# Optimization experiments

Measured on AMD Instinct MI355X. Metric: run time of the kernel, lower is better.

## Reference

```python
import jax, jax.numpy as jnp
import numpy as np

B, S, D, H = 2, 2048, 1024, 16
DK = D // H
NEG = -1e9


def setup_inputs() -> dict:
    key = jax.random.key(0)
    ks = jax.random.split(key, 12)
    scale = 1.0 / np.sqrt(D)
    inp = {
        'Q': jax.random.normal(ks[0], (B, S, D), jnp.float32),
        'K': jax.random.normal(ks[1], (B, S, D), jnp.float32),
        'V': jax.random.normal(ks[2], (B, S, D), jnp.float32),
        'mask': jnp.tril(jnp.ones((S, S), jnp.int32))[None, None],  # (1,1,S,S) causal
        # torch nn.Linear layout: W has shape (out, in), y = x @ W.T + b
        'WQ': jax.random.normal(ks[3], (D, D), jnp.float32) * scale,
        'bQ': jnp.zeros((D,), jnp.float32),
        'WK': jax.random.normal(ks[4], (D, D), jnp.float32) * scale,
        'bK': jnp.zeros((D,), jnp.float32),
        'WV': jax.random.normal(ks[5], (D, D), jnp.float32) * scale,
        'bV': jnp.zeros((D,), jnp.float32),
        'WO': jax.random.normal(ks[6], (D, D), jnp.float32) * scale,
        'bO': jnp.zeros((D,), jnp.float32),
    }
    return inp


def reference(Q, K, V, mask, WQ, bQ, WK, bK, WV, bV, WO, bO):
    # projections (torch Linear: x @ W.T + b), then split heads -> (B,H,S,DK)
    def split_heads(x):
        return x.reshape(B, S, H, DK).transpose(0, 2, 1, 3)

    Qh = split_heads(Q @ WQ.T + bQ)
    Kh = split_heads(K @ WK.T + bK)
    Vh = split_heads(V @ WV.T + bV)

    scores = jnp.einsum('bhqd,bhkd->bhqk', Qh, Kh) / jnp.sqrt(jnp.float32(DK))
    scores = jnp.where(mask == 0, NEG, scores)
    attn = jax.nn.softmax(scores, axis=-1)  # (B,H,S,S)
    ctx = jnp.einsum('bhqk,bhkd->bhqd', attn, Vh)
    concat = ctx.transpose(0, 2, 1, 3).reshape(B, S, D)
    out = concat @ WO.T + bO
    return out, attn
```

## Files before the change

kernel.cpp:

```cpp
#include <hip/hip_runtime.h>
#include <hip/hip_bf16.h>
#include <cstdint>
#include <cstddef>

#define S_ 2048
#define D_ 1024
#define H_ 16
#define DK_ 64
#define B_ 2

typedef unsigned short u16;
typedef __attribute__((ext_vector_type(8))) short bf16x8;
typedef __attribute__((ext_vector_type(4))) float f32x4;

__device__ inline u16 f2bf(float f) {
    union { float f; unsigned u; } c; c.f = f;
    unsigned u = c.u;
    unsigned r = (u + 0x7fffu + ((u >> 16) & 1u)) >> 16;
    return (u16)r;
}

__device__ inline uint4 cvt8(const float* __restrict__ src) {
    float4 f0 = *(const float4*)(src);
    float4 f1 = *(const float4*)(src + 4);
    union { u16 h[8]; uint4 v; } u;
    u.h[0] = f2bf(f0.x); u.h[1] = f2bf(f0.y); u.h[2] = f2bf(f0.z); u.h[3] = f2bf(f0.w);
    u.h[4] = f2bf(f1.x); u.h[5] = f2bf(f1.y); u.h[6] = f2bf(f1.z); u.h[7] = f2bf(f1.w);
    return u.v;
}

__device__ inline unsigned pkbf(float a, float b) {
    unsigned r;
    asm("v_cvt_pk_bf16_f32 %0, %1, %2" : "=v"(r) : "v"(a), "v"(b));
    return r;
}

typedef __attribute__((address_space(3))) void lds_void;
typedef __attribute__((address_space(1))) const void glob_void;
__device__ __forceinline__ void glds16(const u16* g, u16* l, int lane) {
#if __has_builtin(__builtin_amdgcn_global_load_lds)
    (void)lane;
    __builtin_amdgcn_global_load_lds((glob_void*)g, (lds_void*)l, 16, 0, 0);
#else
    ((uint4*)l)[lane] = *(const uint4*)g;
#endif
}

__device__ __forceinline__ bf16x8 rd64(const u16* arr, int row, int k) {
    return *(const bf16x8*)((const char*)arr + (row << 7)
             + ((k << 1) ^ ((row & 7) << 4)));
}
__device__ __forceinline__ bf16x8 rd128(const u16* arr, int row, int k) {
    return *(const bf16x8*)((const char*)arr + (row << 8)
             + ((k << 1) ^ ((row & 7) << 4)));
}

__global__ void __launch_bounds__(256)
cvt_all(const float* __restrict__ Q, const float* __restrict__ K,
        const float* __restrict__ V,
        const float* __restrict__ WQ, const float* __restrict__ WK,
        const float* __restrict__ WV, const float* __restrict__ WO,
        u16* __restrict__ Qb, u16* __restrict__ Kb, u16* __restrict__ Vb,
        u16* __restrict__ Wb)
{
    const size_t QN = 524288;
    const size_t WN = 131072;
    size_t u = (size_t)blockIdx.x * 256 + threadIdx.x;
    const size_t total = 3 * QN + 4 * WN;
    const size_t stride = (size_t)gridDim.x * 256;
    for (; u < total; u += stride) {
        const float* s; u16* d; size_t off;
        if (u < 3 * QN) {
            size_t seg = u / QN;
            off = (u - seg * QN) << 3;
            s = (seg == 0) ? Q : (seg == 1) ? K : V;
            d = (seg == 0) ? Qb : (seg == 1) ? Kb : Vb;
        } else {
            size_t w = u - 3 * QN;
            size_t seg = w / WN;
            off = (w - seg * WN) << 3;
            s = (seg == 0) ? WQ : (seg == 1) ? WK : (seg == 2) ? WV : WO;
            d = Wb + seg * 1048576;
        }
        *(uint4*)&d[off] = cvt8(s + off);
    }
}

__device__ __forceinline__ void gemm_core(
    const u16* __restrict__ A, const u16* __restrict__ Bm,
    int m0, int n0, int tid, u16* As, u16* Bs, f32x4 (&acc)[4][4])
{
    const int lane = tid & 63;
    const int wave = tid >> 6;
    const int wm = wave >> 1, wn = wave & 1;
    const int fr = lane & 15, fq = lane >> 4;

    for (int k0 = 0; k0 < 1024; k0 += 64) {
        __syncthreads();
#pragma unroll
        for (int it = 0; it < 4; ++it) {
            int linear = it * 256 + tid;
            int row = linear >> 3, c = linear & 7;
            glds16(&A[(size_t)(m0 + row) * 1024 + k0 + ((c ^ (row & 7)) << 3)],
                   &As[(size_t)(it * 256 + (tid & ~63)) << 3], lane);
        }
#pragma unroll
        for (int it = 0; it < 4; ++it) {
            int linear = it * 256 + tid;
            int row = linear >> 3, c = linear & 7;
            glds16(&Bm[(size_t)(n0 + row) * 1024 + k0 + ((c ^ (row & 7)) << 3)],
                   &Bs[(size_t)(it * 256 + (tid & ~63)) << 3], lane);
        }
        __syncthreads();
#pragma unroll
        for (int ks = 0; ks < 64; ks += 32) {
            bf16x8 af[4], bfv[4];
#pragma unroll
            for (int mt = 0; mt < 4; ++mt)
                af[mt] = rd64(As, wm * 64 + mt * 16 + fr, ks + (fq << 3));
#pragma unroll
            for (int nt = 0; nt < 4; ++nt)
                bfv[nt] = rd64(Bs, wn * 64 + nt * 16 + fr, ks + (fq << 3));
#pragma unroll
            for (int mt = 0; mt < 4; ++mt)
#pragma unroll
                for (int nt = 0; nt < 4; ++nt)
                    acc[mt][nt] = __builtin_amdgcn_mfma_f32_16x16x32_bf16(
                        bfv[nt], af[mt], acc[mt][nt], 0, 0, 0);
        }
    }
}

__global__ void __launch_bounds__(256)
proj_qkv(const u16* __restrict__ Qb, const u16* __restrict__ Kb,
         const u16* __restrict__ Vb, const u16* __restrict__ Wb,
         const float* __restrict__ bQ, const float* __restrict__ bK,
         const float* __restrict__ bV,
         u16* __restrict__ Qh, u16* __restrict__ Kh, u16* __restrict__ Vt)
{
    __shared__ __align__(16) u16 As[128 * 64];
    __shared__ __align__(16) u16 Bs[128 * 64];

    const int tid  = threadIdx.x;
    const int lane = tid & 63;
    const int wave = tid >> 6;
    const int wm = wave >> 1, wn = wave & 1;
    const int fr = lane & 15, fq = lane >> 4;
    const int m0 = blockIdx.y * 128;
    const int n0 = blockIdx.x * 128;
    const int z  = blockIdx.z;

    const u16* A = (z == 0) ? Qb : (z == 1) ? Kb : Vb;
    const u16* W = Wb + (size_t)z * 1048576;
    const float* bias = (z == 0) ? bQ : (z == 1) ? bK : bV;
    u16* O = (z == 0) ? Qh : (z == 1) ? Kh : Vt;

    f32x4 acc[4][4];
#pragma unroll
    for (int i = 0; i < 4; ++i)
#pragma unroll
        for (int j = 0; j < 4; ++j) acc[i][j] = (f32x4){0.f, 0.f, 0.f, 0.f};

    gemm_core(A, W, m0, n0, tid, As, Bs, acc);

#pragma unroll
    for (int mt = 0; mt < 4; ++mt) {
#pragma unroll
        for (int nt = 0; nt < 4; ++nt) {
            int row  = m0 + wm * 64 + mt * 16 + fr;
            int colb = n0 + wn * 64 + nt * 16 + (fq << 2);
            float4 b4 = *(const float4*)&bias[colb];
            u16 h[4];
            h[0] = f2bf(acc[mt][nt][0] + b4.x);
            h[1] = f2bf(acc[mt][nt][1] + b4.y);
            h[2] = f2bf(acc[mt][nt][2] + b4.z);
            h[3] = f2bf(acc[mt][nt][3] + b4.w);
            if (z < 2) {
                size_t addr = ((size_t)(row >> 11) << 21) + ((size_t)(colb >> 6) << 17)
                            + ((size_t)(row & 2047) << 6) + (size_t)(colb & 63);
                uint2 p; p.x = (unsigned)h[0] | ((unsigned)h[1] << 16);
                         p.y = (unsigned)h[2] | ((unsigned)h[3] << 16);
                *(uint2*)&O[addr] = p;
            } else {
#pragma unroll
                for (int r = 0; r < 4; ++r) {
                    int col = colb + r;
                    size_t addr = ((size_t)(row >> 11) << 21) + ((size_t)(col >> 6) << 17)
                                + ((size_t)(col & 63) << 11) + (size_t)(row & 2047);
                    O[addr] = h[r];
                }
            }
        }
    }
}

__global__ void __launch_bounds__(256)
out_gemm(const u16* __restrict__ Cc, const u16* __restrict__ WOb,
         const float* __restrict__ bO, float* __restrict__ C)
{
    __shared__ __align__(16) u16 As[128 * 64];
    __shared__ __align__(16) u16 Bs[128 * 64];

    const int tid  = threadIdx.x;
    const int lane = tid & 63;
    const int wave = tid >> 6;
    const int wm = wave >> 1, wn = wave & 1;
    const int fr = lane & 15, fq = lane >> 4;
    const int m0 = blockIdx.y * 128;
    const int n0 = blockIdx.x * 128;

    f32x4 acc[4][4];
#pragma unroll
    for (int i = 0; i < 4; ++i)
#pragma unroll
        for (int j = 0; j < 4; ++j) acc[i][j] = (f32x4){0.f, 0.f, 0.f, 0.f};

    gemm_core(Cc, WOb, m0, n0, tid, As, Bs, acc);

#pragma unroll
    for (int mt = 0; mt < 4; ++mt) {
#pragma unroll
        for (int nt = 0; nt < 4; ++nt) {
            int row  = m0 + wm * 64 + mt * 16 + fr;
            int colb = n0 + wn * 64 + nt * 16 + (fq << 2);
            float4 b4 = *(const float4*)&bO[colb];
            float4 v;
            v.x = acc[mt][nt][0] + b4.x;
            v.y = acc[mt][nt][1] + b4.y;
            v.z = acc[mt][nt][2] + b4.z;
            v.w = acc[mt][nt][3] + b4.w;
            *(float4*)&C[(size_t)row * D_ + colb] = v;
        }
    }
}

__global__ void __launch_bounds__(256, 2)
attn_all(const u16* __restrict__ Qh, const u16* __restrict__ Kh,
         const u16* __restrict__ Vt,
         float* __restrict__ attn, u16* __restrict__ Cc)
{
    __shared__ __align__(16) u16 Qs[128 * 64];
    __shared__ __align__(16) u16 Ks[128 * 64];
    __shared__ __align__(16) u16 Vs[64 * 128];
    __shared__ __align__(16) u16 Ps[128 * 128];
    float* rowsum = (float*)Vs;

    const int tid  = threadIdx.x;
    const int lane = tid & 63;
    const int wave = tid >> 6;
    const int wm = wave >> 1, wn = wave & 1;
    const int bx = blockIdx.x;
    const int qt = (bx & 1) ? (15 - (bx >> 1)) : (bx >> 1);
    const int bh = blockIdx.y;
    const int fr = lane & 15, fq = lane >> 4;

    const u16* Qbase = Qh + (size_t)bh * S_ * DK_ + (size_t)qt * 128 * DK_;
    const u16* Kbase = Kh + (size_t)bh * S_ * DK_;
    const u16* Vbase = Vt + (size_t)bh * (size_t)DK_ * S_;
    float* out = attn + (size_t)bh * S_ * S_;

#pragma unroll
    for (int it = 0; it < 4; ++it) {
        int linear = it * 256 + tid;
        int row = linear >> 3, c = linear & 7;
        glds16(&Qbase[(size_t)row * 64 + ((c ^ (row & 7)) << 3)],
               &Qs[(size_t)(it * 256 + (tid & ~63)) << 3], lane);
    }
    if (tid < 128) rowsum[tid] = 0.f;

    float rs[4] = {0.f, 0.f, 0.f, 0.f};

    for (int kt = 0; kt <= qt; ++kt) {
        __syncthreads();
#pragma unroll
        for (int it = 0; it < 4; ++it) {
            int linear = it * 256 + tid;
            int row = linear >> 3, c = linear & 7;
            glds16(&Kbase[(size_t)kt * 128 * 64 + (size_t)row * 64 + ((c ^ (row & 7)) << 3)],
                   &Ks[(size_t)(it * 256 + (tid & ~63)) << 3], lane);
        }
        __syncthreads();

        f32x4 acc[4][4];
#pragma unroll
        for (int i = 0; i < 4; ++i)
#pragma unroll
            for (int j = 0; j < 4; ++j) acc[i][j] = (f32x4){0.f, 0.f, 0.f, 0.f};

#pragma unroll
        for (int ks = 0; ks < 64; ks += 32) {
            bf16x8 kf4[4], qf4[4];
#pragma unroll
            for (int i = 0; i < 4; ++i)
                kf4[i] = rd64(Ks, wm * 64 + i * 16 + fr, ks + (fq << 3));
#pragma unroll
            for (int j = 0; j < 4; ++j)
                qf4[j] = rd64(Qs, wn * 64 + j * 16 + fr, ks + (fq << 3));
#pragma unroll
            for (int i = 0; i < 4; ++i)
#pragma unroll
                for (int j = 0; j < 4; ++j)
                    acc[i][j] = __builtin_amdgcn_mfma_f32_16x16x32_bf16(
                        kf4[i], qf4[j], acc[i][j], 0, 0, 0);
        }

        const bool diag = (kt == qt);
#pragma unroll
        for (int kf = 0; kf < 4; ++kf) {
#pragma unroll
            for (int qf = 0; qf < 4; ++qf) {
                const int kb = wm * 64 + kf * 16, qb = wn * 64 + qf * 16;
                if (!diag || kb < qb) {
#pragma unroll
                    for (int r = 0; r < 4; ++r)
                        rs[qf] += __expf(acc[kf][qf][r] * 0.125f);
                } else if (diag && kb == qb) {
#pragma unroll
                    for (int r = 0; r < 4; ++r)
                        if ((fq << 2) + r <= fr)
                            rs[qf] += __expf(acc[kf][qf][r] * 0.125f);
                }
            }
        }
    }

#pragma unroll
    for (int qf = 0; qf < 4; ++qf) {
        float v = rs[qf];
        v += __shfl_xor(v, 16, 64);
        v += __shfl_xor(v, 32, 64);
        if (lane < 16) atomicAdd(&rowsum[wn * 64 + qf * 16 + lane], v);
    }
    __syncthreads();

    float rcp_l[4];
#pragma unroll
    for (int qf = 0; qf < 4; ++qf)
        rcp_l[qf] = 1.0f / rowsum[wn * 64 + qf * 16 + fr];

    f32x4 cacc[4][2];
#pragma unroll
    for (int i = 0; i < 4; ++i)
#pragma unroll
        for (int j = 0; j < 2; ++j) cacc[i][j] = (f32x4){0.f, 0.f, 0.f, 0.f};

    for (int kt = 0; kt <= qt; ++kt) {
        __syncthreads();
#pragma unroll
        for (int it = 0; it < 4; ++it) {
            int linear = it * 256 + tid;
            int row = linear >> 3, c = linear & 7;
            glds16(&Kbase[(size_t)kt * 128 * 64 + (size_t)row * 64 + ((c ^ (row & 7)) << 3)],
                   &Ks[(size_t)(it * 256 + (tid & ~63)) << 3], lane);
        }
#pragma unroll
        for (int it = 0; it < 4; ++it) {
            int linear = it * 256 + tid;
            int row = linear >> 4, c = linear & 15;
            glds16(&Vbase[(size_t)row * S_ + kt * 128 + ((c ^ (row & 7)) << 3)],
                   &Vs[(size_t)(it * 256 + (tid & ~63)) << 3], lane);
        }
        __syncthreads();

        f32x4 acc[4][4];
#pragma unroll
        for (int i = 0; i < 4; ++i)
#pragma unroll
            for (int j = 0; j < 4; ++j) acc[i][j] = (f32x4){0.f, 0.f, 0.f, 0.f};

#pragma unroll
        for (int ks = 0; ks < 64; ks += 32) {
            bf16x8 kf4[4], qf4[4];
#pragma unroll
            for (int i = 0; i < 4; ++i)
                kf4[i] = rd64(Ks, wm * 64 + i * 16 + fr, ks + (fq << 3));
#pragma unroll
            for (int j = 0; j < 4; ++j)
                qf4[j] = rd64(Qs, wn * 64 + j * 16 + fr, ks + (fq << 3));
#pragma unroll
            for (int i = 0; i < 4; ++i)
#pragma unroll
                for (int j = 0; j < 4; ++j)
                    acc[i][j] = __builtin_amdgcn_mfma_f32_16x16x32_bf16(
                        kf4[i], qf4[j], acc[i][j], 0, 0, 0);
        }

        const bool diag = (kt == qt);
#pragma unroll
        for (int kf = 0; kf < 4; ++kf) {
#pragma unroll
            for (int qf = 0; qf < 4; ++qf) {
                const int kb = wm * 64 + kf * 16, qb = wn * 64 + qf * 16;
                const int qrow = qb + fr;
                float4 p4;
                if (!diag || kb < qb) {
                    p4.x = __expf(acc[kf][qf][0] * 0.125f) * rcp_l[qf];
                    p4.y = __expf(acc[kf][qf][1] * 0.125f) * rcp_l[qf];
                    p4.z = __expf(acc[kf][qf][2] * 0.125f) * rcp_l[qf];
                    p4.w = __expf(acc[kf][qf][3] * 0.125f) * rcp_l[qf];
                } else if (kb > qb) {
                    p4 = (float4){0.f, 0.f, 0.f, 0.f};
                } else {
#pragma unroll
                    for (int r = 0; r < 4; ++r) {
                        float e = __expf(acc[kf][qf][r] * 0.125f) * rcp_l[qf];
                        ((float*)&p4)[r] = ((fq << 2) + r <= fr) ? e : 0.f;
                    }
                }
                *(float4*)&out[(size_t)(qt * 128 + qrow) * S_ + kt * 128 + kb + (fq << 2)] = p4;
                uint2 pk;
                pk.x = pkbf(p4.x, p4.y);
                pk.y = pkbf(p4.z, p4.w);
                *(uint2*)((char*)Ps + (qrow << 8)
                          + (((kb + (fq << 2)) << 1) ^ ((qrow & 7) << 4))) = pk;
            }
        }
        __syncthreads();

#pragma unroll
        for (int ks4 = 0; ks4 < 4; ++ks4) {
            bf16x8 pf[4], vf[2];
            const int kk = ks4 * 32 + (fq << 3);
#pragma unroll
            for (int mt = 0; mt < 4; ++mt)
                pf[mt] = rd128(Ps, wm * 64 + mt * 16 + fr, kk);
#pragma unroll
            for (int nt = 0; nt < 2; ++nt)
                vf[nt] = rd128(Vs, wn * 32 + nt * 16 + fr, kk);
#pragma unroll
            for (int mt = 0; mt < 4; ++mt)
#pragma unroll
                for (int nt = 0; nt < 2; ++nt)
                    cacc[mt][nt] = __builtin_amdgcn_mfma_f32_16x16x32_bf16(
                        pf[mt], vf[nt], cacc[mt][nt], 0, 0, 0);
        }
    }

#pragma unroll
    for (int mt = 0; mt < 4; ++mt)
#pragma unroll
        for (int nt = 0; nt < 2; ++nt)
#pragma unroll
            for (int r = 0; r < 4; ++r) {
                int row = wm * 64 + mt * 16 + (fq << 2) + r;
                int col = wn * 32 + nt * 16 + fr;
                size_t addr = (size_t)(bh >> 4) * S_ * D_ + (size_t)(bh & 15) * DK_
                            + (size_t)(qt * 128 + row) * D_ + col;
                Cc[addr] = f2bf(cacc[mt][nt][r]);
            }

    float4 z4 = {0.f, 0.f, 0.f, 0.f};
    for (int kt2 = qt + 1; kt2 < S_ / 128; ++kt2) {
#pragma unroll
        for (int i = 0; i < 16; ++i) {
            int linear = i * 256 + tid;
            int row = linear >> 5;
            int c   = (linear & 31) << 2;
            *(float4*)&out[(size_t)(qt * 128 + row) * S_ + kt2 * 128 + c] = z4;
        }
    }
}

extern "C" void kernel_launch(void* const* d_in, const int* in_sizes, int n_in,
                              void* d_out, int out_size, void* d_ws, size_t ws_size,
                              hipStream_t stream)
{
    const float* Q  = (const float*)d_in[0];
    const float* K  = (const float*)d_in[1];
    const float* V  = (const float*)d_in[2];
    const float* WQ = (const float*)d_in[4];
    const float* bQ = (const float*)d_in[5];
    const float* WK = (const float*)d_in[6];
    const float* bK = (const float*)d_in[7];
    const float* WV = (const float*)d_in[8];
    const float* bV = (const float*)d_in[9];
    const float* WO = (const float*)d_in[10];
    const float* bO = (const float*)d_in[11];

    float* outF  = (float*)d_out;
    float* attnF = outF + (size_t)B_ * S_ * D_;

    const size_t SZ = (size_t)B_ * S_ * D_;
    u16* Qh = (u16*)d_ws;
    u16* Kh = Qh + SZ;
    u16* Vt = Kh + SZ;
    u16* Cc = Vt + SZ;
    u16* Qb = Cc + SZ;
    u16* Kb = Qb + SZ;
    u16* Vb = Kb + SZ;
    u16* Wb = Vb + SZ;

    dim3 blk(256, 1, 1);

    cvt_all<<<dim3(1024, 1, 1), blk, 0, stream>>>(
        Q, K, V, WQ, WK, WV, WO, Qb, Kb, Vb, Wb);

    proj_qkv<<<dim3(8, 32, 3), blk, 0, stream>>>(
        Qb, Kb, Vb, Wb, bQ, bK, bV, Qh, Kh, Vt);

    attn_all<<<dim3(S_ / 128, B_ * H_, 1), blk, 0, stream>>>(
        Qh, Kh, Vt, attnF, Cc);

    out_gemm<<<dim3(8, 32, 1), blk, 0, stream>>>(
        Cc, Wb + 3 * 1048576, bO, outF);
}
```

Baseline: 771.0 us.

## Double-buffer GEMM LDS tiles and prefetch K/V tiles in attention loops

The projection and output GEMMs now use double-buffered LDS tiles, so the global-to-LDS load for the next k-slice is issued before computing on the current one, with one barrier per iteration. The attention kernel issues the next K (and V) tile load right after the QK^T MFMAs finish, overlapping it with the softmax and PV work instead of loading at the top of each iteration. The causal tile assignment is also changed so half of the heads take reversed q-tile order, which is meant to balance load. GEMM LDS use doubles to 64KB per block, which may reduce occupancy. The attention prefetch into a single buffer adds extra barriers.

```diff
diff --git a/kernel.cpp b/kernel.cpp
--- a/kernel.cpp
+++ b/kernel.cpp
@@ -37,12 +37,11 @@
 
 typedef __attribute__((address_space(3))) void lds_void;
 typedef __attribute__((address_space(1))) const void glob_void;
-__device__ __forceinline__ void glds16(const u16* g, u16* l, int lane) {
+__device__ __forceinline__ void glds16(const u16* g, u16* l) {
 #if __has_builtin(__builtin_amdgcn_global_load_lds)
-    (void)lane;
     __builtin_amdgcn_global_load_lds((glob_void*)g, (lds_void*)l, 16, 0, 0);
 #else
-    ((uint4*)l)[lane] = *(const uint4*)g;
+    ((uint4*)l)[threadIdx.x & 63] = *(const uint4*)g;
 #endif
 }
 
@@ -86,6 +85,21 @@
     }
 }
 
+__device__ __forceinline__ void gemm_stage(
+    const u16* __restrict__ A, const u16* __restrict__ Bm,
+    int m0, int n0, int k0, int tid, u16* As, u16* Bs)
+{
+#pragma unroll
+    for (int it = 0; it < 4; ++it) {
+        int linear = it * 256 + tid;
+        int row = linear >> 3, c = linear & 7;
+        glds16(&A[(size_t)(m0 + row) * 1024 + k0 + ((c ^ (row & 7)) << 3)],
+               &As[(size_t)(it * 256 + (tid & ~63)) << 3]);
+        glds16(&Bm[(size_t)(n0 + row) * 1024 + k0 + ((c ^ (row & 7)) << 3)],
+               &Bs[(size_t)(it * 256 + (tid & ~63)) << 3]);
+    }
+}
+
 __device__ __forceinline__ void gemm_core(
     const u16* __restrict__ A, const u16* __restrict__ Bm,
     int m0, int n0, int tid, u16* As, u16* Bs, f32x4 (&acc)[4][4])
@@ -95,32 +109,25 @@
     const int wm = wave >> 1, wn = wave & 1;
     const int fr = lane & 15, fq = lane >> 4;
 
-    for (int k0 = 0; k0 < 1024; k0 += 64) {
-        __syncthreads();
-#pragma unroll
-        for (int it = 0; it < 4; ++it) {
-            int linear = it * 256 + tid;
-            int row = linear >> 3, c = linear & 7;
-            glds16(&A[(size_t)(m0 + row) * 1024 + k0 + ((c ^ (row & 7)) << 3)],
-                   &As[(size_t)(it * 256 + (tid & ~63)) << 3], lane);
-        }
-#pragma unroll
-        for (int it = 0; it < 4; ++it) {
-            int linear = it * 256 + tid;
-            int row = linear >> 3, c = linear & 7;
-            glds16(&Bm[(size_t)(n0 + row) * 1024 + k0 + ((c ^ (row & 7)) << 3)],
-                   &Bs[(size_t)(it * 256 + (tid & ~63)) << 3], lane);
-        }
-        __syncthreads();
+    gemm_stage(A, Bm, m0, n0, 0, tid, As, Bs);
+    __syncthreads();
+
+    for (int t = 0; t < 16; ++t) {
+        const int cur = t & 1;
+        u16* Ac = As + cur * 8192;
+        u16* Bc = Bs + cur * 8192;
+        if (t + 1 < 16)
+            gemm_stage(A, Bm, m0, n0, (t + 1) * 64, tid,
+                       As + (cur ^ 1) * 8192, Bs + (cur ^ 1) * 8192);
 #pragma unroll
         for (int ks = 0; ks < 64; ks += 32) {
             bf16x8 af[4], bfv[4];
 #pragma unroll
             for (int mt = 0; mt < 4; ++mt)
-                af[mt] = rd64(As, wm * 64 + mt * 16 + fr, ks + (fq << 3));
+                af[mt] = rd64(Ac, wm * 64 + mt * 16 + fr, ks + (fq << 3));
 #pragma unroll
             for (int nt = 0; nt < 4; ++nt)
-                bfv[nt] = rd64(Bs, wn * 64 + nt * 16 + fr, ks + (fq << 3));
+                bfv[nt] = rd64(Bc, wn * 64 + nt * 16 + fr, ks + (fq << 3));
 #pragma unroll
             for (int mt = 0; mt < 4; ++mt)
 #pragma unroll
@@ -128,6 +135,7 @@
                     acc[mt][nt] = __builtin_amdgcn_mfma_f32_16x16x32_bf16(
                         bfv[nt], af[mt], acc[mt][nt], 0, 0, 0);
         }
+        __syncthreads();
     }
 }
 
@@ -138,8 +146,8 @@
          const float* __restrict__ bV,
          u16* __restrict__ Qh, u16* __restrict__ Kh, u16* __restrict__ Vt)
 {
-    __shared__ __align__(16) u16 As[128 * 64];
-    __shared__ __align__(16) u16 Bs[128 * 64];
+    __shared__ __align__(16) u16 As[2 * 128 * 64];
+    __shared__ __align__(16) u16 Bs[2 * 128 * 64];
 
     const int tid  = threadIdx.x;
     const int lane = tid & 63;
@@ -198,8 +206,8 @@
 out_gemm(const u16* __restrict__ Cc, const u16* __restrict__ WOb,
          const float* __restrict__ bO, float* __restrict__ C)
 {
-    __shared__ __align__(16) u16 As[128 * 64];
-    __shared__ __align__(16) u16 Bs[128 * 64];
+    __shared__ __align__(16) u16 As[2 * 128 * 64];
+    __shared__ __align__(16) u16 Bs[2 * 128 * 64];
 
     const int tid  = threadIdx.x;
     const int lane = tid & 63;
@@ -250,8 +258,8 @@
     const int wave = tid >> 6;
     const int wm = wave >> 1, wn = wave & 1;
     const int bx = blockIdx.x;
-    const int qt = (bx & 1) ? (15 - (bx >> 1)) : (bx >> 1);
     const int bh = blockIdx.y;
+    const int qt = (bh & 16) ? (15 - bx) : bx;
     const int fr = lane & 15, fq = lane >> 4;
 
     const u16* Qbase = Qh + (size_t)bh * S_ * DK_ + (size_t)qt * 128 * DK_;
@@ -264,23 +272,16 @@
         int linear = it * 256 + tid;
         int row = linear >> 3, c = linear & 7;
         glds16(&Qbase[(size_t)row * 64 + ((c ^ (row & 7)) << 3)],
-               &Qs[(size_t)(it * 256 + (tid & ~63)) << 3], lane);
+               &Qs[(size_t)(it * 256 + (tid & ~63)) << 3]);
+        glds16(&Kbase[(size_t)row * 64 + ((c ^ (row & 7)) << 3)],
+               &Ks[(size_t)(it * 256 + (tid & ~63)) << 3]);
     }
     if (tid < 128) rowsum[tid] = 0.f;
+    __syncthreads();
 
     float rs[4] = {0.f, 0.f, 0.f, 0.f};
 
     for (int kt = 0; kt <= qt; ++kt) {
-        __syncthreads();
-#pragma unroll
-        for (int it = 0; it < 4; ++it) {
-            int linear = it * 256 + tid;
-            int row = linear >> 3, c = linear & 7;
-            glds16(&Kbase[(size_t)kt * 128 * 64 + (size_t)row * 64 + ((c ^ (row & 7)) << 3)],
-                   &Ks[(size_t)(it * 256 + (tid & ~63)) << 3], lane);
-        }
-        __syncthreads();
-
         f32x4 acc[4][4];
 #pragma unroll
         for (int i = 0; i < 4; ++i)
@@ -302,6 +303,17 @@
                 for (int j = 0; j < 4; ++j)
                     acc[i][j] = __builtin_amdgcn_mfma_f32_16x16x32_bf16(
                         kf4[i], qf4[j], acc[i][j], 0, 0, 0);
+        }
+        __syncthreads();
+        if (kt < qt) {
+#pragma unroll
+            for (int it = 0; it < 4; ++it) {
+                int linear = it * 256 + tid;
+                int row = linear >> 3, c = linear & 7;
+                glds16(&Kbase[(size_t)(kt + 1) * 128 * 64 + (size_t)row * 64
+                              + ((c ^ (row & 7)) << 3)],
+                       &Ks[(size_t)(it * 256 + (tid & ~63)) << 3]);
+            }
         }
 
         const bool diag = (kt == qt);
@@ -322,6 +334,7 @@
                 }
             }
         }
+        __syncthreads();
     }
 
 #pragma unroll
@@ -337,6 +350,7 @@
 #pragma unroll
     for (int qf = 0; qf < 4; ++qf)
         rcp_l[qf] = 1.0f / rowsum[wn * 64 + qf * 16 + fr];
+    __syncthreads();
 
     f32x4 cacc[4][2];
 #pragma unroll
@@ -344,24 +358,19 @@
 #pragma unroll
         for (int j = 0; j < 2; ++j) cacc[i][j] = (f32x4){0.f, 0.f, 0.f, 0.f};
 
+#pragma unroll
+    for (int it = 0; it < 4; ++it) {
+        int linear = it * 256 + tid;
+        int row = linear >> 3, c = linear & 7;
+        glds16(&Kbase[(size_t)row * 64 + ((c ^ (row & 7)) << 3)],
+               &Ks[(size_t)(it * 256 + (tid & ~63)) << 3]);
+        int rv = linear >> 4, cv = linear & 15;
+        glds16(&Vbase[(size_t)rv * S_ + ((cv ^ (rv & 7)) << 3)],
+               &Vs[(size_t)(it * 256 + (tid & ~63)) << 3]);
+    }
+    __syncthreads();
+
     for (int kt = 0; kt <= qt; ++kt) {
-        __syncthreads();
-#pragma unroll
-        for (int it = 0; it < 4; ++it) {
-            int linear = it * 256 + tid;
-            int row = linear >> 3, c = linear & 7;
-            glds16(&Kbase[(size_t)kt * 128 * 64 + (size_t)row * 64 + ((c ^ (row & 7)) << 3)],
-                   &Ks[(size_t)(it * 256 + (tid & ~63)) << 3], lane);
-        }
-#pragma unroll
-        for (int it = 0; it < 4; ++it) {
-            int linear = it * 256 + tid;
-            int row = linear >> 4, c = linear & 15;
-            glds16(&Vbase[(size_t)row * S_ + kt * 128 + ((c ^ (row & 7)) << 3)],
-                   &Vs[(size_t)(it * 256 + (tid & ~63)) << 3], lane);
-        }
-        __syncthreads();
-
         f32x4 acc[4][4];
 #pragma unroll
         for (int i = 0; i < 4; ++i)
@@ -383,6 +392,17 @@
                 for (int j = 0; j < 4; ++j)
                     acc[i][j] = __builtin_amdgcn_mfma_f32_16x16x32_bf16(
                         kf4[i], qf4[j], acc[i][j], 0, 0, 0);
+        }
+        __syncthreads();
+        if (kt < qt) {
+#pragma unroll
+            for (int it = 0; it < 4; ++it) {
+                int linear = it * 256 + tid;
+                int row = linear >> 3, c = linear & 7;
+                glds16(&Kbase[(size_t)(kt + 1) * 128 * 64 + (size_t)row * 64
+                              + ((c ^ (row & 7)) << 3)],
+                       &Ks[(size_t)(it * 256 + (tid & ~63)) << 3]);
+            }
         }
 
         const bool diag = (kt == qt);
@@ -434,6 +454,16 @@
                     cacc[mt][nt] = __builtin_amdgcn_mfma_f32_16x16x32_bf16(
                         pf[mt], vf[nt], cacc[mt][nt], 0, 0, 0);
         }
+        __syncthreads();
+        if (kt < qt) {
+#pragma unroll
+            for (int it = 0; it < 4; ++it) {
+                int linear = it * 256 + tid;
+                int rv = linear >> 4, cv = linear & 15;
+                glds16(&Vbase[(size_t)rv * S_ + (kt + 1) * 128 + ((cv ^ (rv & 7)) << 3)],
+                       &Vs[(size_t)(it * 256 + (tid & ~63)) << 3]);
+            }
+        }
     }
 
 #pragma unroll
```

Result: no change. 774.0 us (+0.4%).
